# Kernel tuning notes

Measured on AMD Instinct MI355X. Metric: run time of the kernel, lower is better.

Reference implementation:

```python
import jax, jax.numpy as jnp
import numpy as np

LN_EPS = 1e-6  # flax.linen.LayerNorm default

def _layernorm(x, scale, bias):
    mu = jnp.mean(x, axis=-1, keepdims=True)
    var = jnp.mean(jnp.square(x - mu), axis=-1, keepdims=True)
    return (x - mu) * jax.lax.rsqrt(var + LN_EPS) * scale + bias

def setup_inputs() -> dict:
    key = jax.random.key(0)
    ks = jax.random.split(key, 16)
    N, D = 65536, 512
    W = 1024  # hidden width for all 4 layers
    def init_w(k, fan_in, fan_out):
        # lecun_normal (flax Dense default kernel init)
        return jax.random.normal(k, (fan_in, fan_out), jnp.float32) / np.sqrt(fan_in)
    return {
        "descriptors": jax.random.normal(ks[0], (N, D), jnp.float32),
        "W0": init_w(ks[1], D, W),
        "b0": jnp.zeros((W,), jnp.float32),
        "W1": init_w(ks[2], W, W),
        "g1": jnp.ones((W,), jnp.float32),
        "be1": jnp.zeros((W,), jnp.float32),
        "W2": init_w(ks[3], W, W),
        "g2": jnp.ones((W,), jnp.float32),
        "be2": jnp.zeros((W,), jnp.float32),
        "W3": init_w(ks[4], W, W),
        "g3": jnp.ones((W,), jnp.float32),
        "be3": jnp.zeros((W,), jnp.float32),
        "Wout": init_w(ks[5], W, 1),
        "bout": jnp.zeros((1,), jnp.float32),
    }

def reference(descriptors, W0, b0, W1, g1, be1, W2, g2, be2, W3, g3, be3, Wout, bout):
    # layer 0: Dense (with bias) -> relu
    h = jax.nn.relu(descriptors @ W0 + b0)  # [N, 1024]
    # hidden layers: bias-free Dense -> LayerNorm -> relu
    for Wk, gk, bk in ((W1, g1, be1), (W2, g2, be2), (W3, g3, be3)):
        h = jax.nn.relu(_layernorm(h @ Wk, gk, bk))
    # output: Dense(1) with bias -> relu
    return jax.nn.relu(h @ Wout + bout)  # [N, 1]
```

## Files before the change

kernel.cpp:

```cpp
#include <hip/hip_runtime.h>

typedef _Float16 f16;
typedef _Float16 f16x8 __attribute__((ext_vector_type(8)));
typedef float f32x4 __attribute__((ext_vector_type(4)));

#define TILE 128
#define BK 32

__device__ __forceinline__ void async_cp16(const void* g, void* l) {
  __builtin_amdgcn_global_load_lds(
      (const __attribute__((address_space(1))) void*)g,
      (__attribute__((address_space(3))) void*)l, 16, 0, 0);
}

template <int EPI>
__global__ __launch_bounds__(256) void gemm_f16(
    const f16* __restrict__ A, const f16* __restrict__ Bt,
    const float* __restrict__ bias, f16* __restrict__ C,
    int M, int N, int K) {
  __shared__ alignas(16) f16 sA[TILE][BK];
  __shared__ alignas(16) f16 sB[TILE][BK];
  const int tid = threadIdx.x;
  const int lane = tid & 63;
  const int wave = tid >> 6;

  int mt, nt;
  if (gridDim.x == 8 && gridDim.y == 512) {
    const int id = blockIdx.y * 8 + blockIdx.x;
    nt = (id >> 3) & 7;
    mt = (id & 7) * 64 + (id >> 6);
  } else {
    nt = blockIdx.x;
    mt = blockIdx.y;
  }
  const long long bm = (long long)mt * TILE;
  const long long bn = (long long)nt * TILE;

  const int wm = (wave & 1) * 64;
  const int wn = (wave >> 1) * 64;
  const int r15 = lane & 15;
  const int quad = lane >> 4;
  const int qsw = ((r15 >> 1) & 3);

  f32x4 acc[4][4] = {};

  const int kIters = K / BK;
  for (int kt = 0; kt < kIters; ++kt) {
    const int k0 = kt * BK;
#pragma unroll
    for (int i = 0; i < 2; ++i) {
      const int chunk = wave * 128 + i * 64 + lane;
      const int ml = chunk >> 2;
      const int kc = (chunk & 3) ^ ((ml >> 1) & 3);
      async_cp16(A + (bm + ml) * (long long)K + k0 + kc * 8,
                 &sA[0][0] + (long long)(wave * 128 + i * 64) * 8);
      async_cp16(Bt + (bn + ml) * (long long)K + k0 + kc * 8,
                 &sB[0][0] + (long long)(wave * 128 + i * 64) * 8);
    }
    __syncthreads();

    f16x8 af[4], bf[4];
#pragma unroll
    for (int i = 0; i < 4; ++i) {
      af[i] = *(const f16x8*)&sA[wm + i * 16 + r15][(quad ^ qsw) * 8];
      bf[i] = *(const f16x8*)&sB[wn + i * 16 + r15][(quad ^ qsw) * 8];
    }
#pragma unroll
    for (int i = 0; i < 4; ++i)
#pragma unroll
      for (int j = 0; j < 4; ++j)
        acc[i][j] =
            __builtin_amdgcn_mfma_f32_16x16x32_f16(af[i], bf[j], acc[i][j], 0, 0, 0);
    __syncthreads();
  }

#pragma unroll
  for (int j = 0; j < 4; ++j) {
    const long long colg = bn + wn + j * 16 + r15;
    float bval = 0.f;
    if (EPI == 0) bval = bias[colg];
#pragma unroll
    for (int i = 0; i < 4; ++i) {
#pragma unroll
      for (int r = 0; r < 4; ++r) {
        const long long rowg = bm + wm + i * 16 + quad * 4 + r;
        float v = acc[i][j][r];
        if (EPI == 0) v = fmaxf(v + bval, 0.f);
        C[rowg * N + colg] = (f16)v;
      }
    }
  }
}

__global__ __launch_bounds__(256) void ln_relu_kernel(
    const f16* __restrict__ Y, const float* __restrict__ g,
    const float* __restrict__ b, f16* __restrict__ H) {
  const int lane = threadIdx.x & 63;
  const int wave = threadIdx.x >> 6;
  const long long row = (long long)blockIdx.x * 4 + wave;
  const f16* y = Y + row * 1024;
  float x[16];
  float s1 = 0.f, s2 = 0.f;
#pragma unroll
  for (int p = 0; p < 2; ++p) {
    f16x8 v = *(const f16x8*)(y + p * 512 + lane * 8);
#pragma unroll
    for (int e = 0; e < 8; ++e) {
      const float f = (float)v[e];
      x[p * 8 + e] = f;
      s1 += f;
      s2 += f * f;
    }
  }
#pragma unroll
  for (int off = 32; off >= 1; off >>= 1) {
    s1 += __shfl_xor(s1, off);
    s2 += __shfl_xor(s2, off);
  }
  const float mean = s1 * (1.f / 1024.f);
  const float var = fmaxf(s2 * (1.f / 1024.f) - mean * mean, 0.f);
  const float inv = rsqrtf(var + 1e-6f);
  f16* h = H + row * 1024;
#pragma unroll
  for (int p = 0; p < 2; ++p) {
    f16x8 o;
#pragma unroll
    for (int e = 0; e < 8; ++e) {
      const int c = p * 512 + lane * 8 + e;
      const float v = (x[p * 8 + e] - mean) * inv * g[c] + b[c];
      o[e] = (f16)fmaxf(v, 0.f);
    }
    *(f16x8*)(h + p * 512 + lane * 8) = o;
  }
}

__global__ __launch_bounds__(256) void ln_relu_out_kernel(
    const f16* __restrict__ Y, const float* __restrict__ g,
    const float* __restrict__ b, const float* __restrict__ Wout,
    const float* __restrict__ bout, float* __restrict__ out) {
  const int lane = threadIdx.x & 63;
  const int wave = threadIdx.x >> 6;
  const long long row = (long long)blockIdx.x * 4 + wave;
  const f16* y = Y + row * 1024;
  float x[16];
  float s1 = 0.f, s2 = 0.f;
#pragma unroll
  for (int p = 0; p < 2; ++p) {
    f16x8 v = *(const f16x8*)(y + p * 512 + lane * 8);
#pragma unroll
    for (int e = 0; e < 8; ++e) {
      const float f = (float)v[e];
      x[p * 8 + e] = f;
      s1 += f;
      s2 += f * f;
    }
  }
#pragma unroll
  for (int off = 32; off >= 1; off >>= 1) {
    s1 += __shfl_xor(s1, off);
    s2 += __shfl_xor(s2, off);
  }
  const float mean = s1 * (1.f / 1024.f);
  const float var = fmaxf(s2 * (1.f / 1024.f) - mean * mean, 0.f);
  const float inv = rsqrtf(var + 1e-6f);
  float dot = 0.f;
#pragma unroll
  for (int p = 0; p < 2; ++p) {
#pragma unroll
    for (int e = 0; e < 8; ++e) {
      const int c = p * 512 + lane * 8 + e;
      const float v = fmaxf((x[p * 8 + e] - mean) * inv * g[c] + b[c], 0.f);
      dot += v * Wout[c];
    }
  }
#pragma unroll
  for (int off = 32; off >= 1; off >>= 1) dot += __shfl_xor(dot, off);
  if (lane == 0) out[row] = fmaxf(dot + bout[0], 0.f);
}

__global__ __launch_bounds__(256) void cvt_f16_kernel(const float* __restrict__ X,
                                                      f16* __restrict__ Y,
                                                      long long n) {
  const long long i = ((long long)blockIdx.x * 256 + threadIdx.x) * 8;
  if (i >= n) return;
  const float4* X4 = (const float4*)(X + i);
  const float4 a = X4[0], c = X4[1];
  f16x8 o;
  o[0] = (f16)a.x; o[1] = (f16)a.y; o[2] = (f16)a.z; o[3] = (f16)a.w;
  o[4] = (f16)c.x; o[5] = (f16)c.y; o[6] = (f16)c.z; o[7] = (f16)c.w;
  *(f16x8*)(Y + i) = o;
}

__global__ __launch_bounds__(256) void transpose_cvt(const float* __restrict__ W,
                                                     f16* __restrict__ Wt, int K,
                                                     int N) {
  __shared__ float tile[64][65];
  const int bn = blockIdx.x * 64;
  const int bk = blockIdx.y * 64;
  const int tx = threadIdx.x & 63;
  const int ty = threadIdx.x >> 6;
#pragma unroll
  for (int i = 0; i < 64; i += 4)
    tile[ty + i][tx] = W[(long long)(bk + ty + i) * N + bn + tx];
  __syncthreads();
#pragma unroll
  for (int i = 0; i < 64; i += 4)
    Wt[(long long)(bn + ty + i) * K + bk + tx] = (f16)tile[tx][ty + i];
}

extern "C" void kernel_launch(void* const* d_in, const int* in_sizes, int n_in,
                              void* d_out, int out_size, void* d_ws, size_t ws_size,
                              hipStream_t stream) {
  const float* desc = (const float*)d_in[0];
  const float* W0 = (const float*)d_in[1];
  const float* b0 = (const float*)d_in[2];
  const float* W1 = (const float*)d_in[3];
  const float* g1 = (const float*)d_in[4];
  const float* be1 = (const float*)d_in[5];
  const float* W2 = (const float*)d_in[6];
  const float* g2 = (const float*)d_in[7];
  const float* be2 = (const float*)d_in[8];
  const float* W3 = (const float*)d_in[9];
  const float* g3 = (const float*)d_in[10];
  const float* be3 = (const float*)d_in[11];
  const float* Wout = (const float*)d_in[12];
  const float* bout = (const float*)d_in[13];
  float* out = (float*)d_out;

  const long long Nrows = 65536, D = 512, W = 1024;
  char* p = (char*)d_ws;
  f16* descH = (f16*)p; p += Nrows * D * sizeof(f16);
  f16* Wt0 = (f16*)p;   p += D * W * sizeof(f16);
  f16* Wt1 = (f16*)p;   p += W * W * sizeof(f16);
  f16* Wt2 = (f16*)p;   p += W * W * sizeof(f16);
  f16* Wt3 = (f16*)p;   p += W * W * sizeof(f16);
  f16* H = (f16*)p;     p += Nrows * W * sizeof(f16);
  f16* Y = (f16*)p;     p += Nrows * W * sizeof(f16);
  (void)ws_size; (void)in_sizes; (void)n_in; (void)out_size;

  cvt_f16_kernel<<<(int)(Nrows * D / 8 / 256), 256, 0, stream>>>(desc, descH,
                                                                 Nrows * D);
  transpose_cvt<<<dim3(W / 64, D / 64), 256, 0, stream>>>(W0, Wt0, (int)D, (int)W);
  transpose_cvt<<<dim3(W / 64, W / 64), 256, 0, stream>>>(W1, Wt1, (int)W, (int)W);
  transpose_cvt<<<dim3(W / 64, W / 64), 256, 0, stream>>>(W2, Wt2, (int)W, (int)W);
  transpose_cvt<<<dim3(W / 64, W / 64), 256, 0, stream>>>(W3, Wt3, (int)W, (int)W);

  dim3 ggrid(W / TILE, Nrows / TILE);
  gemm_f16<0><<<ggrid, 256, 0, stream>>>(descH, Wt0, b0, H, (int)Nrows, (int)W, (int)D);

  gemm_f16<1><<<ggrid, 256, 0, stream>>>(H, Wt1, nullptr, Y, (int)Nrows, (int)W, (int)W);
  ln_relu_kernel<<<(int)(Nrows / 4), 256, 0, stream>>>(Y, g1, be1, H);

  gemm_f16<1><<<ggrid, 256, 0, stream>>>(H, Wt2, nullptr, Y, (int)Nrows, (int)W, (int)W);
  ln_relu_kernel<<<(int)(Nrows / 4), 256, 0, stream>>>(Y, g2, be2, H);

  gemm_f16<1><<<ggrid, 256, 0, stream>>>(H, Wt3, nullptr, Y, (int)Nrows, (int)W, (int)W);
  ln_relu_out_kernel<<<(int)(Nrows / 4), 256, 0, stream>>>(Y, g3, be3, Wout, bout, out);
}
```

Baseline: 1.046 ms.

## Switch GEMM to 32x32x16 MFMA with BK=64 and precomputed load pointers

Replaces the 16x16x32 MFMA tiling with 32x32x16 MFMA (2x2 per wave, f32x16 accumulators) and doubles the K tile to 64, with an 8-way XOR swizzle on the LDS layout. Global source pointers are computed once and advanced each iteration instead of recomputing addresses. The aim is to cut LDS read traffic per FLOP and halve the number of barrier pairs. The cost is a larger LDS footprint per block and a different epilogue row mapping.

```diff
diff --git a/kernel.cpp b/kernel.cpp
--- a/kernel.cpp
+++ b/kernel.cpp
@@ -2,10 +2,10 @@
 
 typedef _Float16 f16;
 typedef _Float16 f16x8 __attribute__((ext_vector_type(8)));
-typedef float f32x4 __attribute__((ext_vector_type(4)));
+typedef float f32x16 __attribute__((ext_vector_type(16)));
 
 #define TILE 128
-#define BK 32
+#define BK 64
 
 __device__ __forceinline__ void async_cp16(const void* g, void* l) {
   __builtin_amdgcn_global_load_lds(
@@ -38,58 +38,66 @@
 
   const int wm = (wave & 1) * 64;
   const int wn = (wave >> 1) * 64;
-  const int r15 = lane & 15;
-  const int quad = lane >> 4;
-  const int qsw = ((r15 >> 1) & 3);
-
-  f32x4 acc[4][4] = {};
+  const int l31 = lane & 31;
+  const int half = lane >> 5;
+
+  const f16 *aSrc[4], *bSrc[4];
+#pragma unroll
+  for (int i = 0; i < 4; ++i) {
+    const int chunk = wave * 256 + i * 64 + lane;
+    const int ml = chunk >> 3;
+    const int kc = (chunk & 7) ^ (ml & 7);
+    aSrc[i] = A + (bm + ml) * (long long)K + kc * 8;
+    bSrc[i] = Bt + (bn + ml) * (long long)K + kc * 8;
+  }
+
+  f32x16 acc[2][2] = {};
 
   const int kIters = K / BK;
   for (int kt = 0; kt < kIters; ++kt) {
-    const int k0 = kt * BK;
-#pragma unroll
-    for (int i = 0; i < 2; ++i) {
-      const int chunk = wave * 128 + i * 64 + lane;
-      const int ml = chunk >> 2;
-      const int kc = (chunk & 3) ^ ((ml >> 1) & 3);
-      async_cp16(A + (bm + ml) * (long long)K + k0 + kc * 8,
-                 &sA[0][0] + (long long)(wave * 128 + i * 64) * 8);
-      async_cp16(Bt + (bn + ml) * (long long)K + k0 + kc * 8,
-                 &sB[0][0] + (long long)(wave * 128 + i * 64) * 8);
+#pragma unroll
+    for (int i = 0; i < 4; ++i) {
+      async_cp16(aSrc[i], &sA[0][0] + (long long)(wave * 256 + i * 64) * 8);
+      async_cp16(bSrc[i], &sB[0][0] + (long long)(wave * 256 + i * 64) * 8);
+      aSrc[i] += BK;
+      bSrc[i] += BK;
     }
     __syncthreads();
 
-    f16x8 af[4], bf[4];
-#pragma unroll
-    for (int i = 0; i < 4; ++i) {
-      af[i] = *(const f16x8*)&sA[wm + i * 16 + r15][(quad ^ qsw) * 8];
-      bf[i] = *(const f16x8*)&sB[wn + i * 16 + r15][(quad ^ qsw) * 8];
-    }
-#pragma unroll
-    for (int i = 0; i < 4; ++i)
-#pragma unroll
-      for (int j = 0; j < 4; ++j)
-        acc[i][j] =
-            __builtin_amdgcn_mfma_f32_16x16x32_f16(af[i], bf[j], acc[i][j], 0, 0, 0);
+#pragma unroll
+    for (int s = 0; s < 4; ++s) {
+      const int csw = ((s * 2 + half) ^ (lane & 7)) * 8;
+      f16x8 af[2], bf[2];
+#pragma unroll
+      for (int i = 0; i < 2; ++i) af[i] = *(const f16x8*)&sA[wm + i * 32 + l31][csw];
+#pragma unroll
+      for (int j = 0; j < 2; ++j) bf[j] = *(const f16x8*)&sB[wn + j * 32 + l31][csw];
+#pragma unroll
+      for (int i = 0; i < 2; ++i)
+#pragma unroll
+        for (int j = 0; j < 2; ++j)
+          acc[i][j] = __builtin_amdgcn_mfma_f32_32x32x16_f16(af[i], bf[j],
+                                                             acc[i][j], 0, 0, 0);
+    }
     __syncthreads();
   }
 
 #pragma unroll
-  for (int j = 0; j < 4; ++j) {
-    const long long colg = bn + wn + j * 16 + r15;
-    float bval = 0.f;
-    if (EPI == 0) bval = bias[colg];
-#pragma unroll
-    for (int i = 0; i < 4; ++i) {
-#pragma unroll
-      for (int r = 0; r < 4; ++r) {
-        const long long rowg = bm + wm + i * 16 + quad * 4 + r;
-        float v = acc[i][j][r];
+  for (int i = 0; i < 2; ++i)
+#pragma unroll
+    for (int j = 0; j < 2; ++j) {
+      const long long colg = bn + wn + j * 32 + l31;
+      float bval = 0.f;
+      if (EPI == 0) bval = bias[colg];
+#pragma unroll
+      for (int reg = 0; reg < 16; ++reg) {
+        const long long rowg =
+            bm + wm + i * 32 + (reg & 3) + 8 * (reg >> 2) + 4 * half;
+        float v = acc[i][j][reg];
         if (EPI == 0) v = fmaxf(v + bval, 0.f);
         C[rowg * N + colg] = (f16)v;
       }
     }
-  }
 }
 
 __global__ __launch_bounds__(256) void ln_relu_kernel(
```

After: 921.5 us. -11.9%, faster.
